# Performance work log

Measured on AMD Instinct MI355X. Metric: run time of the kernel, lower is better.

## Reference

```python
import jax, jax.numpy as jnp
import numpy as np

B, N, C, H = 4, 2048, 384, 6
D = C // H                       # head_dim = 64
HID = 4 * C                      # mlp hidden = 1536
SCALE = D ** -0.5
EPS = 1e-5                       # torch nn.LayerNorm default


def setup_inputs() -> dict:
    key = jax.random.key(0)
    ks = jax.random.split(key, 8)
    s = 0.02
    return {
        "x": jax.random.normal(ks[0], (B, N, C), jnp.float32),
        "ln1_g": jnp.ones((C,), jnp.float32),
        "ln1_b": jnp.zeros((C,), jnp.float32),
        "w_qkv": jax.random.normal(ks[1], (3 * C, C), jnp.float32) * s,
        "w_proj": jax.random.normal(ks[2], (C, C), jnp.float32) * s,
        "b_proj": jnp.zeros((C,), jnp.float32),
        "ln2_g": jnp.ones((C,), jnp.float32),
        "ln2_b": jnp.zeros((C,), jnp.float32),
        "w_fc1": jax.random.normal(ks[3], (HID, C), jnp.float32) * s,
        "b_fc1": jnp.zeros((HID,), jnp.float32),
        "w_fc2": jax.random.normal(ks[4], (C, HID), jnp.float32) * s,
        "b_fc2": jnp.zeros((C,), jnp.float32),
    }


def _layernorm(x, g, b):
    mu = jnp.mean(x, axis=-1, keepdims=True)
    var = jnp.mean(jnp.square(x - mu), axis=-1, keepdims=True)
    return (x - mu) * jax.lax.rsqrt(var + EPS) * g + b


def _bf16_round(x):
    # emulate the .bfloat16() cast after each residual (precision truncation)
    return x.astype(jnp.bfloat16).astype(jnp.float32)


def reference(x, ln1_g, ln1_b, w_qkv, w_proj, b_proj,
              ln2_g, ln2_b, w_fc1, b_fc1, w_fc2, b_fc2):
    # ---- attention branch (quant=False => HMQ ops are pass-through) ----
    h = _layernorm(x, ln1_g, ln1_b)                       # [B,N,C]
    qkv = jnp.einsum('bnc,oc->bno', h, w_qkv)             # [B,N,3C]
    qkv = qkv.reshape(B, N, 3, H, D).transpose(2, 0, 3, 1, 4)  # [3,B,H,N,D]
    q, k, v = qkv[0], qkv[1], qkv[2]
    attn = jnp.einsum('bhnd,bhmd->bhnm', q, k) * SCALE    # [B,H,N,N]
    attn = jax.nn.softmax(attn, axis=-1)
    o = jnp.einsum('bhnm,bhmd->bhnd', attn, v)            # [B,H,N,D]
    o = o.transpose(0, 2, 1, 3).reshape(B, N, C)
    o = jnp.einsum('bnc,oc->bno', o, w_proj) + b_proj
    x = _bf16_round(x + o)

    # ---- MLP branch ----
    h = _layernorm(x, ln2_g, ln2_b)
    h = jnp.einsum('bnc,hc->bnh', h, w_fc1) + b_fc1       # [B,N,HID]
    h = jax.nn.gelu(h, approximate=False)
    h = jnp.einsum('bnh,ch->bnc', h, w_fc2) + b_fc2       # [B,N,C]
    x = _bf16_round(x + h)
    return x
```

## Files before the change

kernel.cpp:

```cpp
#include <hip/hip_runtime.h>
#include <cstdint>
#include <cstddef>

#define DI __device__ __forceinline__

typedef __attribute__((ext_vector_type(8))) short short8;
typedef __attribute__((ext_vector_type(4))) float f32x4;
typedef unsigned int u32;
typedef unsigned short u16;

DI u16 rne_bf16(float f) {
  union { float f; u32 u; } v; v.f = f;
  u32 b = v.u;
  return (u16)((b + 0x7fffu + ((b >> 16) & 1u)) >> 16);
}
DI float bf2f(u16 h) {
  union { u32 u; float f; } v; v.u = ((u32)h) << 16;
  return v.f;
}
DI u32 cvtpk_bf16(float a, float b) {
  u32 r;
  asm("v_cvt_pk_bf16_f32 %0, %1, %2" : "=v"(r) : "v"(a), "v"(b));
  return r;
}

DI void gl2lds16(const void* g, void* l) {
  __builtin_amdgcn_global_load_lds(
      (const __attribute__((address_space(1))) u32*)g,
      (__attribute__((address_space(3))) u32*)l, 16, 0, 0);
}

DI void bar() {
  asm volatile("" ::: "memory");
  __builtin_amdgcn_s_barrier();
  asm volatile("" ::: "memory");
}

template<int ROWS, int NT>
DI void stage_swz(const u16* src, int ld, char* ldsb, int tid) {
  int wbase = tid & ~63;
  #pragma unroll
  for (int c = 0; c < (ROWS * 8) / NT; ++c) {
    int g = c * NT + tid;
    int row = g >> 3;
    int sgr = (g & 7) ^ (row & 7);
    gl2lds16(src + row * ld + sgr * 8, ldsb + (size_t)(c * NT + wbase) * 16);
  }
}

DI short8 lds_frag(const char* base, int row, int k0) {
  return *(const short8*)(base + row * 128 + ((k0 * 2) ^ ((row & 7) << 4)));
}

DI f32x4 mfma16(short8 a, short8 b, f32x4 c) {
  return __builtin_amdgcn_mfma_f32_16x16x32_bf16(a, b, c, 0, 0, 0);
}

__global__ __launch_bounds__(256) void cvt_w(
    const float* __restrict__ a, const float* __restrict__ b,
    const float* __restrict__ c, const float* __restrict__ d,
    u16* __restrict__ oa, u16* __restrict__ ob, u16* __restrict__ oc,
    u16* __restrict__ od) {
  int i = blockIdx.x * 256 + threadIdx.x;
  if (i < 442368) oa[i] = rne_bf16(a[i]);
  else if (i < 589824) ob[i - 442368] = rne_bf16(b[i - 442368]);
  else if (i < 1179648) oc[i - 589824] = rne_bf16(c[i - 589824]);
  else if (i < 1769472) od[i - 1179648] = rne_bf16(d[i - 1179648]);
}

template<int INBF>
__global__ __launch_bounds__(256) void ln_k(
    const void* __restrict__ xin, const float* __restrict__ gam,
    const float* __restrict__ bet, u16* __restrict__ out) {
  int row = blockIdx.x * 4 + (threadIdx.x >> 6);
  int lane = threadIdx.x & 63;
  float v[6];
  if (INBF) {
    const u16* x = (const u16*)xin + (size_t)row * 384 + lane;
    #pragma unroll
    for (int j = 0; j < 6; ++j) v[j] = bf2f(x[j * 64]);
  } else {
    const float* x = (const float*)xin + (size_t)row * 384 + lane;
    #pragma unroll
    for (int j = 0; j < 6; ++j) v[j] = x[j * 64];
  }
  float s = 0.f;
  #pragma unroll
  for (int j = 0; j < 6; ++j) s += v[j];
  #pragma unroll
  for (int d = 1; d < 64; d <<= 1) s += __shfl_xor(s, d);
  float mu = s * (1.f / 384.f);
  float q = 0.f;
  #pragma unroll
  for (int j = 0; j < 6; ++j) { float t = v[j] - mu; q += t * t; }
  #pragma unroll
  for (int d = 1; d < 64; d <<= 1) q += __shfl_xor(q, d);
  float rstd = rsqrtf(q * (1.f / 384.f) + 1e-5f);
  #pragma unroll
  for (int j = 0; j < 6; ++j) {
    int c = j * 64 + lane;
    out[(size_t)row * 384 + c] = rne_bf16((v[j] - mu) * rstd * gam[c] + bet[c]);
  }
}

struct EpiP {
  const float* bias;
  const float* residf;
  const u16* residb;
  u16* outb;
  float* outf;
  u16* q; u16* k; u16* v;
};

#define QSCALE 0.18033688011112042f

template<int EPI, int MT>
__global__ __launch_bounds__(256) void gemm_bt(
    const u16* __restrict__ A, const u16* __restrict__ W, int K, int bnN,
    EpiP p) {
  constexpr int ABUF = MT * 128;
  constexpr int NC = (MT == 128) ? 4 : 2;
  __shared__ char lds[2 * (ABUF + 16384)];
  int tid = threadIdx.x, lane = tid & 63, wid = tid >> 6;
  int wr = (MT == 128) ? (wid >> 1) * 64 : 0;
  int wcb = (MT == 128) ? (wid & 1) * 64 : wid * 32;
  int fr = lane & 15, k8 = lane >> 4;
  int orig = blockIdx.x;
  int cpx = (int)gridDim.x >> 3;
  int wg = (orig & 7) * cpx + (orig >> 3);
  int bm = wg / bnN, bn = wg - bm * bnN;
  const u16* Ab = A + (size_t)bm * MT * K;
  const u16* Wb = W + (size_t)bn * 128 * K;

  stage_swz<MT, 256>(Ab, K, lds, tid);
  stage_swz<128, 256>(Wb, K, lds + ABUF, tid);

  f32x4 zz = {0.f, 0.f, 0.f, 0.f};
  f32x4 acc[4][NC];
  #pragma unroll
  for (int mr = 0; mr < 4; ++mr)
    #pragma unroll
    for (int nc = 0; nc < NC; ++nc) acc[mr][nc] = zz;

  asm volatile("s_waitcnt vmcnt(0)" ::: "memory");
  __syncthreads();

  int KT = K >> 6;
  for (int t = 0; t < KT; ++t) {
    char* base = lds + (size_t)(t & 1) * (ABUF + 16384);
    if (t + 1 < KT) {
      char* nb = lds + (size_t)((t + 1) & 1) * (ABUF + 16384);
      stage_swz<MT, 256>(Ab + (t + 1) * 64, K, nb, tid);
      stage_swz<128, 256>(Wb + (t + 1) * 64, K, nb + ABUF, tid);
    }
    #pragma unroll
    for (int ks = 0; ks < 2; ++ks) {
      int k0 = ks * 32 + k8 * 8;
      short8 av[4], bv[NC];
      #pragma unroll
      for (int mr = 0; mr < 4; ++mr) av[mr] = lds_frag(base, wr + mr * 16 + fr, k0);
      #pragma unroll
      for (int nc = 0; nc < NC; ++nc) bv[nc] = lds_frag(base + ABUF, wcb + nc * 16 + fr, k0);
      __builtin_amdgcn_s_setprio(1);
      #pragma unroll
      for (int mr = 0; mr < 4; ++mr)
        #pragma unroll
        for (int nc = 0; nc < NC; ++nc)
          acc[mr][nc] = mfma16(av[mr], bv[nc], acc[mr][nc]);
      __builtin_amdgcn_s_setprio(0);
    }
    asm volatile("s_waitcnt vmcnt(0)" ::: "memory");
    __syncthreads();
  }

  #pragma unroll
  for (int mr = 0; mr < 4; ++mr)
    #pragma unroll
    for (int nc = 0; nc < NC; ++nc)
      #pragma unroll
      for (int r = 0; r < 4; ++r) {
        int m = bm * MT + wr + mr * 16 + k8 * 4 + r;
        int o = bn * 128 + wcb + nc * 16 + fr;
        float val = acc[mr][nc][r];
        if constexpr (EPI == 0) {
          int tq = o / 384;
          int rem = o - tq * 384;
          int hh = rem >> 6, d = rem & 63;
          int b = m >> 11, n = m & 2047;
          float sv = (tq == 0) ? val * QSCALE : val;
          u16 bvs = rne_bf16(sv);
          size_t qk = (((size_t)(b * 6 + hh)) * 2048 + n) * 64 + d;
          if (tq == 0) p.q[qk] = bvs;
          else if (tq == 1) p.k[qk] = bvs;
          else p.v[qk] = bvs;
        } else if constexpr (EPI == 1) {
          size_t idx = (size_t)m * 384 + o;
          float r2 = p.residf[idx] + val + p.bias[o];
          p.outb[idx] = rne_bf16(r2);
        } else if constexpr (EPI == 2) {
          size_t idx = (size_t)m * 1536 + o;
          float z = val + p.bias[o];
          float gl = 0.5f * z * (1.f + erff(z * 0.70710678118654752f));
          p.outb[idx] = rne_bf16(gl);
        } else {
          size_t idx = (size_t)m * 384 + o;
          float r2 = bf2f(p.residb[idx]) + val + p.bias[o];
          p.outf[idx] = bf2f(rne_bf16(r2));
        }
      }
}

__global__ __launch_bounds__(256) void vtr_k(
    const u16* __restrict__ v, u16* __restrict__ vt) {
  __shared__ u16 t[64 * 74];
  int tid = threadIdx.x;
  int n0 = blockIdx.x * 64, bh = blockIdx.y;
  const u16* src = v + ((size_t)bh * 2048 + n0) * 64;
  #pragma unroll
  for (int it = 0; it < 2; ++it) {
    int row = it * 32 + (tid >> 3), c8 = tid & 7;
    *(short8*)&t[row * 74 + c8 * 8] = *(const short8*)(src + row * 64 + c8 * 8);
  }
  __syncthreads();
  int dp = tid >> 3;
  int ng = tid & 7;
  u16 lo[8], hi[8];
  #pragma unroll
  for (int j = 0; j < 8; ++j) {
    u32 a = *(const u32*)&t[(ng * 8 + j) * 74 + dp * 2];
    lo[j] = (u16)a; hi[j] = (u16)(a >> 16);
  }
  u16* dst = vt + ((size_t)bh * 64 + 2 * dp) * 2048 + n0 + ng * 8;
  *(short8*)dst = *(short8*)&lo[0];
  *(short8*)(dst + 2048) = *(short8*)&hi[0];
}

__global__ __launch_bounds__(256) void attn_k(
    const u16* __restrict__ Qg, const u16* __restrict__ Kg,
    const u16* __restrict__ Vg, float* __restrict__ Op, float* __restrict__ lp) {
  __shared__ char lds[51712];
  int tid = threadIdx.x, lane = tid & 63, wid = tid >> 6;
  int fr = lane & 15, k8 = lane >> 4;
  int qt = blockIdx.x, bh = blockIdx.y, z = blockIdx.z;
  const u16* Qb = Qg + (size_t)bh * 2048 * 64;
  const u16* Kb = Kg + ((size_t)bh * 2048 + z * 1024) * 64;
  const u16* Vb = Vg + (size_t)bh * 64 * 2048 + z * 1024;
  int qr0 = qt * 128 + wid * 32;

  short8 qf[2][2];
  #pragma unroll
  for (int mr = 0; mr < 2; ++mr)
    #pragma unroll
    for (int ks = 0; ks < 2; ++ks)
      qf[mr][ks] = *(const short8*)(Qb + (size_t)(qr0 + mr * 16 + fr) * 64 + ks * 32 + k8 * 8);

  short8 ones;
  #pragma unroll
  for (int i = 0; i < 8; ++i) ones[i] = (short)0x3F80;

  f32x4 zz = {0.f, 0.f, 0.f, 0.f};
  f32x4 oacc[2][4], lacc[2];
  #pragma unroll
  for (int mr = 0; mr < 2; ++mr) {
    #pragma unroll
    for (int nc = 0; nc < 4; ++nc) oacc[mr][nc] = zz;
    lacc[mr] = zz;
  }
  char* P = lds + 32768 + wid * 4736;

  #define STAGE(t)                                                              \
    stage_swz<64, 256>(Kb + (size_t)(t) * 4096, 64, lds + ((t) & 1) * 8192, tid); \
    stage_swz<64, 256>(Vb + (t) * 64, 2048, lds + 16384 + ((t) & 1) * 8192, tid);

  STAGE(0);
  asm volatile("s_waitcnt vmcnt(0)" ::: "memory");
  bar();

  for (int t = 0; t < 16; ++t) {
    if (t + 1 < 16) { STAGE(t + 1); }
    char* kbase = lds + (t & 1) * 8192;
    char* vbase = lds + 16384 + (t & 1) * 8192;
    f32x4 s[2][4];
    #pragma unroll
    for (int mr = 0; mr < 2; ++mr)
      #pragma unroll
      for (int nc = 0; nc < 4; ++nc) s[mr][nc] = zz;
    #pragma unroll
    for (int ks = 0; ks < 2; ++ks) {
      int k0 = ks * 32 + k8 * 8;
      short8 kf[4];
      #pragma unroll
      for (int nc = 0; nc < 4; ++nc) kf[nc] = lds_frag(kbase, nc * 16 + fr, k0);
      __builtin_amdgcn_s_setprio(1);
      #pragma unroll
      for (int mr = 0; mr < 2; ++mr)
        #pragma unroll
        for (int nc = 0; nc < 4; ++nc)
          s[mr][nc] = mfma16(qf[mr][ks], kf[nc], s[mr][nc]);
      __builtin_amdgcn_s_setprio(0);
    }
    #pragma unroll
    for (int mr = 0; mr < 2; ++mr)
      #pragma unroll
      for (int nc = 0; nc < 4; ++nc)
        #pragma unroll
        for (int rp = 0; rp < 2; ++rp) {
          float p0 = exp2f(s[mr][nc][2 * rp]);
          float p1 = exp2f(s[mr][nc][2 * rp + 1]);
          u32 w = cvtpk_bf16(p0, p1);
          char* base = P + (mr * 16 + k8 * 4 + 2 * rp) * 148 + (nc * 16 + fr) * 2;
          *(u16*)base = (u16)w;
          *(u16*)(base + 148) = (u16)(w >> 16);
        }
    #pragma unroll
    for (int ks = 0; ks < 2; ++ks) {
      int k0 = ks * 32 + k8 * 8;
      short8 pa[2], vf[4];
      #pragma unroll
      for (int mr = 0; mr < 2; ++mr)
        pa[mr] = *(const short8*)(P + (mr * 16 + fr) * 148 + k0 * 2);
      #pragma unroll
      for (int nc = 0; nc < 4; ++nc) vf[nc] = lds_frag(vbase, nc * 16 + fr, k0);
      __builtin_amdgcn_s_setprio(1);
      #pragma unroll
      for (int mr = 0; mr < 2; ++mr) {
        #pragma unroll
        for (int nc = 0; nc < 4; ++nc)
          oacc[mr][nc] = mfma16(pa[mr], vf[nc], oacc[mr][nc]);
        lacc[mr] = mfma16(pa[mr], ones, lacc[mr]);
      }
      __builtin_amdgcn_s_setprio(0);
    }
    asm volatile("s_waitcnt vmcnt(0)" ::: "memory");
    if (t < 15) bar();
  }
  #undef STAGE

  size_t rowb = (size_t)z * 49152 + (size_t)bh * 2048;
  #pragma unroll
  for (int mr = 0; mr < 2; ++mr)
    #pragma unroll
    for (int nc = 0; nc < 4; ++nc)
      #pragma unroll
      for (int r = 0; r < 4; ++r) {
        int qrow = qr0 + mr * 16 + k8 * 4 + r;
        Op[(rowb + qrow) * 64 + nc * 16 + fr] = oacc[mr][nc][r];
      }
  if (fr == 0)
    #pragma unroll
    for (int mr = 0; mr < 2; ++mr)
      #pragma unroll
      for (int r = 0; r < 4; ++r)
        lp[rowb + qr0 + mr * 16 + k8 * 4 + r] = lacc[mr][r];
}

__global__ __launch_bounds__(256) void attn_merge(
    const float* __restrict__ Op, const float* __restrict__ lp,
    u16* __restrict__ ao) {
  int row = blockIdx.x * 4 + (threadIdx.x >> 6);
  int d = threadIdx.x & 63;
  float l = lp[row] + lp[49152 + row];
  float v = (Op[(size_t)row * 64 + d] + Op[(size_t)(49152 + row) * 64 + d]) / l;
  int bh = row >> 11, n = row & 2047;
  int b = bh / 6, hh = bh - b * 6;
  ao[((size_t)(b * 2048 + n)) * 384 + hh * 64 + d] = rne_bf16(v);
}

extern "C" void kernel_launch(void* const* d_in, const int* in_sizes, int n_in,
                              void* d_out, int out_size, void* d_ws, size_t ws_size,
                              hipStream_t stream) {
  const float* x     = (const float*)d_in[0];
  const float* ln1g  = (const float*)d_in[1];
  const float* ln1b  = (const float*)d_in[2];
  const float* wqkv  = (const float*)d_in[3];
  const float* wproj = (const float*)d_in[4];
  const float* bproj = (const float*)d_in[5];
  const float* ln2g  = (const float*)d_in[6];
  const float* ln2b  = (const float*)d_in[7];
  const float* wfc1  = (const float*)d_in[8];
  const float* bfc1  = (const float*)d_in[9];
  const float* wfc2  = (const float*)d_in[10];
  const float* bfc2  = (const float*)d_in[11];
  float* out = (float*)d_out;

  char* w = (char*)d_ws;
  u16* h1     = (u16*)w; w += 6291456;
  u16* x2     = (u16*)w; w += 6291456;
  u16* h2     = (u16*)w; w += 6291456;
  u16* qb     = (u16*)w; w += 6291456;
  u16* kb     = (u16*)w; w += 6291456;
  u16* vtb    = (u16*)w; w += 6291456;
  u16* ao     = (u16*)w; w += 6291456;
  u16* act    = (u16*)w; w += 25165824;
  u16* wqkvb  = (u16*)w; w += 884736;
  u16* wprojb = (u16*)w; w += 294912;
  u16* wfc1b  = (u16*)w; w += 1179648;
  u16* wfc2b  = (u16*)w; w += 1179648;

  u16* v_nat   = h2;
  float* Opart = (float*)act;
  float* lpart = (float*)h2;

  cvt_w<<<6912, 256, 0, stream>>>(wqkv, wproj, wfc1, wfc2, wqkvb, wprojb, wfc1b, wfc2b);
  ln_k<0><<<2048, 256, 0, stream>>>(x, ln1g, ln1b, h1);
  {
    EpiP p{}; p.q = qb; p.k = kb; p.v = v_nat;
    gemm_bt<0, 64><<<1152, 256, 0, stream>>>(h1, wqkvb, 384, 9, p);
  }
  vtr_k<<<dim3(32, 24), 256, 0, stream>>>(v_nat, vtb);
  attn_k<<<dim3(16, 24, 2), 256, 0, stream>>>(qb, kb, vtb, Opart, lpart);
  attn_merge<<<12288, 256, 0, stream>>>(Opart, lpart, ao);
  {
    EpiP p{}; p.bias = bproj; p.residf = x; p.outb = x2;
    gemm_bt<1, 64><<<384, 256, 0, stream>>>(ao, wprojb, 384, 3, p);
  }
  ln_k<1><<<2048, 256, 0, stream>>>(x2, ln2g, ln2b, h2);
  {
    EpiP p{}; p.bias = bfc1; p.outb = act;
    gemm_bt<2, 128><<<768, 256, 0, stream>>>(h2, wfc1b, 384, 12, p);
  }
  {
    EpiP p{}; p.bias = bfc2; p.residb = x2; p.outf = out;
    gemm_bt<3, 64><<<384, 256, 0, stream>>>(act, wfc2b, 1536, 3, p);
  }
}
```

Baseline: 241.6 us.

## Rewrite attention with 32x32 MFMA, computing S transposed to keep P in registers

Attention now uses 32x32x16 bf16 MFMAs and computes S transposed (K as the A operand, Q as B). Each lane then holds the probabilities for one query column, so P can be converted to the A-operand layout with lane shuffles across the half-wave instead of a round trip through LDS. The row sum is accumulated in VALU rather than with a ones-vector MFMA, and the per-wave P scratch in LDS is removed, which cuts LDS use. The GEMM also skips its wait and barrier after the last K tile. This adds shuffle and select work and depends on the transposed-layout index mapping being correct.

```diff
diff --git a/kernel.cpp b/kernel.cpp
--- a/kernel.cpp
+++ b/kernel.cpp
@@ -6,6 +6,7 @@
 
 typedef __attribute__((ext_vector_type(8))) short short8;
 typedef __attribute__((ext_vector_type(4))) float f32x4;
+typedef __attribute__((ext_vector_type(16))) float f32x16;
 typedef unsigned int u32;
 typedef unsigned short u16;
 
@@ -54,6 +55,9 @@
 
 DI f32x4 mfma16(short8 a, short8 b, f32x4 c) {
   return __builtin_amdgcn_mfma_f32_16x16x32_bf16(a, b, c, 0, 0, 0);
+}
+DI f32x16 mfma32(short8 a, short8 b, f32x16 c) {
+  return __builtin_amdgcn_mfma_f32_32x32x16_bf16(a, b, c, 0, 0, 0);
 }
 
 __global__ __launch_bounds__(256) void cvt_w(
@@ -169,8 +173,10 @@
           acc[mr][nc] = mfma16(av[mr], bv[nc], acc[mr][nc]);
       __builtin_amdgcn_s_setprio(0);
     }
-    asm volatile("s_waitcnt vmcnt(0)" ::: "memory");
-    __syncthreads();
+    if (t + 1 < KT) {
+      asm volatile("s_waitcnt vmcnt(0)" ::: "memory");
+      __syncthreads();
+    }
   }
 
   #pragma unroll
@@ -238,35 +244,26 @@
 __global__ __launch_bounds__(256) void attn_k(
     const u16* __restrict__ Qg, const u16* __restrict__ Kg,
     const u16* __restrict__ Vg, float* __restrict__ Op, float* __restrict__ lp) {
-  __shared__ char lds[51712];
+  __shared__ char lds[32768];
   int tid = threadIdx.x, lane = tid & 63, wid = tid >> 6;
-  int fr = lane & 15, k8 = lane >> 4;
+  int l31 = lane & 31, h = lane >> 5;
   int qt = blockIdx.x, bh = blockIdx.y, z = blockIdx.z;
   const u16* Qb = Qg + (size_t)bh * 2048 * 64;
   const u16* Kb = Kg + ((size_t)bh * 2048 + z * 1024) * 64;
   const u16* Vb = Vg + (size_t)bh * 64 * 2048 + z * 1024;
   int qr0 = qt * 128 + wid * 32;
 
-  short8 qf[2][2];
-  #pragma unroll
-  for (int mr = 0; mr < 2; ++mr)
-    #pragma unroll
-    for (int ks = 0; ks < 2; ++ks)
-      qf[mr][ks] = *(const short8*)(Qb + (size_t)(qr0 + mr * 16 + fr) * 64 + ks * 32 + k8 * 8);
-
-  short8 ones;
-  #pragma unroll
-  for (int i = 0; i < 8; ++i) ones[i] = (short)0x3F80;
-
-  f32x4 zz = {0.f, 0.f, 0.f, 0.f};
-  f32x4 oacc[2][4], lacc[2];
-  #pragma unroll
-  for (int mr = 0; mr < 2; ++mr) {
-    #pragma unroll
-    for (int nc = 0; nc < 4; ++nc) oacc[mr][nc] = zz;
-    lacc[mr] = zz;
-  }
-  char* P = lds + 32768 + wid * 4736;
+  short8 qf[4];
+  #pragma unroll
+  for (int m = 0; m < 4; ++m)
+    qf[m] = *(const short8*)(Qb + (size_t)(qr0 + l31) * 64 + m * 16 + h * 8);
+
+  f32x16 oacc[2];
+  #pragma unroll
+  for (int dt = 0; dt < 2; ++dt)
+    #pragma unroll
+    for (int r = 0; r < 16; ++r) oacc[dt][r] = 0.f;
+  float lrun = 0.f;
 
   #define STAGE(t)                                                              \
     stage_swz<64, 256>(Kb + (size_t)(t) * 4096, 64, lds + ((t) & 1) * 8192, tid); \
@@ -280,78 +277,73 @@
     if (t + 1 < 16) { STAGE(t + 1); }
     char* kbase = lds + (t & 1) * 8192;
     char* vbase = lds + 16384 + (t & 1) * 8192;
-    f32x4 s[2][4];
-    #pragma unroll
-    for (int mr = 0; mr < 2; ++mr)
-      #pragma unroll
-      for (int nc = 0; nc < 4; ++nc) s[mr][nc] = zz;
-    #pragma unroll
-    for (int ks = 0; ks < 2; ++ks) {
-      int k0 = ks * 32 + k8 * 8;
+
+    f32x16 s[2];
+    #pragma unroll
+    for (int kt = 0; kt < 2; ++kt) {
+      #pragma unroll
+      for (int r = 0; r < 16; ++r) s[kt][r] = 0.f;
       short8 kf[4];
       #pragma unroll
-      for (int nc = 0; nc < 4; ++nc) kf[nc] = lds_frag(kbase, nc * 16 + fr, k0);
+      for (int m = 0; m < 4; ++m)
+        kf[m] = lds_frag(kbase, kt * 32 + l31, m * 16 + h * 8);
       __builtin_amdgcn_s_setprio(1);
       #pragma unroll
-      for (int mr = 0; mr < 2; ++mr)
-        #pragma unroll
-        for (int nc = 0; nc < 4; ++nc)
-          s[mr][nc] = mfma16(qf[mr][ks], kf[nc], s[mr][nc]);
+      for (int m = 0; m < 4; ++m) s[kt] = mfma32(kf[m], qf[m], s[kt]);
       __builtin_amdgcn_s_setprio(0);
     }
     #pragma unroll
-    for (int mr = 0; mr < 2; ++mr)
-      #pragma unroll
-      for (int nc = 0; nc < 4; ++nc)
-        #pragma unroll
-        for (int rp = 0; rp < 2; ++rp) {
-          float p0 = exp2f(s[mr][nc][2 * rp]);
-          float p1 = exp2f(s[mr][nc][2 * rp + 1]);
-          u32 w = cvtpk_bf16(p0, p1);
-          char* base = P + (mr * 16 + k8 * 4 + 2 * rp) * 148 + (nc * 16 + fr) * 2;
-          *(u16*)base = (u16)w;
-          *(u16*)(base + 148) = (u16)(w >> 16);
-        }
-    #pragma unroll
-    for (int ks = 0; ks < 2; ++ks) {
-      int k0 = ks * 32 + k8 * 8;
-      short8 pa[2], vf[4];
-      #pragma unroll
-      for (int mr = 0; mr < 2; ++mr)
-        pa[mr] = *(const short8*)(P + (mr * 16 + fr) * 148 + k0 * 2);
-      #pragma unroll
-      for (int nc = 0; nc < 4; ++nc) vf[nc] = lds_frag(vbase, nc * 16 + fr, k0);
-      __builtin_amdgcn_s_setprio(1);
-      #pragma unroll
-      for (int mr = 0; mr < 2; ++mr) {
-        #pragma unroll
-        for (int nc = 0; nc < 4; ++nc)
-          oacc[mr][nc] = mfma16(pa[mr], vf[nc], oacc[mr][nc]);
-        lacc[mr] = mfma16(pa[mr], ones, lacc[mr]);
+    for (int kt = 0; kt < 2; ++kt)
+      #pragma unroll
+      for (int r = 0; r < 16; ++r) {
+        float pv = exp2f(s[kt][r]);
+        s[kt][r] = pv;
+        lrun += pv;
       }
-      __builtin_amdgcn_s_setprio(0);
+    #pragma unroll
+    for (int kt = 0; kt < 2; ++kt) {
+      u32 ow[4][2], pw[4][2];
+      #pragma unroll
+      for (int B = 0; B < 4; ++B) {
+        ow[B][0] = cvtpk_bf16(s[kt][4 * B + 0], s[kt][4 * B + 1]);
+        ow[B][1] = cvtpk_bf16(s[kt][4 * B + 2], s[kt][4 * B + 3]);
+      }
+      #pragma unroll
+      for (int B = 0; B < 4; ++B) {
+        pw[B][0] = __shfl_xor(ow[B][0], 32);
+        pw[B][1] = __shfl_xor(ow[B][1], 32);
+      }
+      #pragma unroll
+      for (int m = 0; m < 2; ++m) {
+        union { u32 w[4]; short8 v; } af;
+        af.w[0] = h ? pw[2 * m + 1][0] : ow[2 * m][0];
+        af.w[1] = h ? pw[2 * m + 1][1] : ow[2 * m][1];
+        af.w[2] = h ? ow[2 * m + 1][0] : pw[2 * m][0];
+        af.w[3] = h ? ow[2 * m + 1][1] : pw[2 * m][1];
+        int K0 = kt * 32 + m * 16;
+        short8 vf0 = lds_frag(vbase, l31, K0 + h * 8);
+        short8 vf1 = lds_frag(vbase, 32 + l31, K0 + h * 8);
+        __builtin_amdgcn_s_setprio(1);
+        oacc[0] = mfma32(af.v, vf0, oacc[0]);
+        oacc[1] = mfma32(af.v, vf1, oacc[1]);
+        __builtin_amdgcn_s_setprio(0);
+      }
     }
     asm volatile("s_waitcnt vmcnt(0)" ::: "memory");
     if (t < 15) bar();
   }
   #undef STAGE
 
+  float ltot = lrun + __shfl_xor(lrun, 32);
   size_t rowb = (size_t)z * 49152 + (size_t)bh * 2048;
   #pragma unroll
-  for (int mr = 0; mr < 2; ++mr)
-    #pragma unroll
-    for (int nc = 0; nc < 4; ++nc)
-      #pragma unroll
-      for (int r = 0; r < 4; ++r) {
-        int qrow = qr0 + mr * 16 + k8 * 4 + r;
-        Op[(rowb + qrow) * 64 + nc * 16 + fr] = oacc[mr][nc][r];
-      }
-  if (fr == 0)
-    #pragma unroll
-    for (int mr = 0; mr < 2; ++mr)
-      #pragma unroll
-      for (int r = 0; r < 4; ++r)
-        lp[rowb + qr0 + mr * 16 + k8 * 4 + r] = lacc[mr][r];
+  for (int dt = 0; dt < 2; ++dt)
+    #pragma unroll
+    for (int r = 0; r < 16; ++r) {
+      int qrow = qr0 + (r & 3) + 8 * (r >> 2) + 4 * h;
+      Op[(rowb + qrow) * 64 + dt * 32 + l31] = oacc[dt][r];
+    }
+  if (lane < 32) lp[rowb + qr0 + l31] = ltot;
 }
 
 __global__ __launch_bounds__(256) void attn_merge(
```

New measurement: 228.9 us. -5.3%, faster.
